# Optimization experiments

Hardware: AMD Instinct MI355X
Metric: run time of the kernel (lower is better)

## Reference

```python
import jax, jax.numpy as jnp
import numpy as np

M_PER_GROUP = 16
EPS = 0.001


def setup_inputs() -> dict:
    key = jax.random.key(0)
    x = jax.random.normal(key, (32, 64, 64, 256), dtype=jnp.float32)
    return {"x": x}


def reference(x) -> jnp.ndarray:
    # x: [B, W, H, C] (NHWC). Training-phase path, decomposition='cholesky', renorm=False.
    b, w, h, c = x.shape
    groups = c // M_PER_GROUP
    n = b * w * h  # samples per channel

    # [C, B*W*H]
    x_flat = jnp.transpose(x, (3, 0, 1, 2)).reshape(c, -1)
    mean = jnp.mean(x_flat, axis=1, keepdims=True)          # [C, 1]
    f = x_flat - mean                                        # [C, N]

    # per-group covariance: [G, m, N] -> [G, m, m]
    fg = f.reshape(groups, M_PER_GROUP, -1)
    denom = jnp.float32(n) - 1.0
    cov = jnp.einsum('gmn,gkn->gmk', fg, fg) / denom
    eye = jnp.eye(M_PER_GROUP, dtype=x.dtype)
    cov = (1.0 - EPS) * cov + EPS * eye
    # NOTE: the original TF code divides by (N-1) a second time after shrinkage;
    # reproduced faithfully here.
    cov = cov / denom

    # batched Cholesky + triangular solve: inv_sqrt = L^{-1}
    chol = jnp.linalg.cholesky(cov)                          # [G, m, m], lower
    inv_sqrt = jax.vmap(
        lambda L: jax.scipy.linalg.solve_triangular(L, eye, lower=True)
    )(chol)                                                  # [G, m, m]

    # whiten: [G, m, m] @ [G, m, N] -> [G, m, N]
    f_hat = jnp.einsum('gmk,gkn->gmn', inv_sqrt, fg)
    out = f_hat.reshape(c, b, w, h)
    return jnp.transpose(out, (1, 2, 3, 0))
```

## Files before the change

kernel.cpp:

```cpp
#include <hip/hip_runtime.h>


#define NROWS   131072
#define DENOMF  131071.0f
#define EPSV    0.001f

#define OFF_INV    0
#define OFF_BIAS   4096
#define OFF_RED1   4352
#define OFF_PART4  217344
#define GSTATS     13312

typedef __attribute__((ext_vector_type(8))) short bf16x8;
typedef __attribute__((ext_vector_type(4))) float f32x4;
typedef __attribute__((ext_vector_type(4))) unsigned int u32x4;

__device__ __forceinline__ unsigned int fbits(float v) {
    return __builtin_bit_cast(unsigned int, v);
}
__device__ __forceinline__ float bfloat(unsigned int u) {
    return __builtin_bit_cast(float, u);
}

__device__ __forceinline__ void gload_lds16(float* lds, const float* g) {
    __builtin_amdgcn_global_load_lds(
        (const __attribute__((address_space(1))) unsigned int*)g,
        (__attribute__((address_space(3))) unsigned int*)lds, 16, 0, 0);
}

struct Row8 { float a, b, c, d, e, f, g, h; };

__device__ __forceinline__ void cvt8(const Row8 r, bf16x8& hv, bf16x8& lv, float& s) {
    s += ((r.a + r.b) + (r.c + r.d)) + ((r.e + r.f) + (r.g + r.h));
    const unsigned int ua = fbits(r.a), ub = fbits(r.b), uc = fbits(r.c), ud = fbits(r.d);
    const unsigned int ue = fbits(r.e), uf = fbits(r.f), ug = fbits(r.g), uh = fbits(r.h);
    u32x4 hp;
    hp.x = (ub & 0xFFFF0000u) | (ua >> 16);
    hp.y = (ud & 0xFFFF0000u) | (uc >> 16);
    hp.z = (uf & 0xFFFF0000u) | (ue >> 16);
    hp.w = (uh & 0xFFFF0000u) | (ug >> 16);
    const float da = r.a - bfloat(ua & 0xFFFF0000u);
    const float db = r.b - bfloat(ub & 0xFFFF0000u);
    const float dc = r.c - bfloat(uc & 0xFFFF0000u);
    const float dd = r.d - bfloat(ud & 0xFFFF0000u);
    const float de = r.e - bfloat(ue & 0xFFFF0000u);
    const float df = r.f - bfloat(uf & 0xFFFF0000u);
    const float dg = r.g - bfloat(ug & 0xFFFF0000u);
    const float dh = r.h - bfloat(uh & 0xFFFF0000u);
    u32x4 lp;
    lp.x = (fbits(db) & 0xFFFF0000u) | (fbits(da) >> 16);
    lp.y = (fbits(dd) & 0xFFFF0000u) | (fbits(dc) >> 16);
    lp.z = (fbits(df) & 0xFFFF0000u) | (fbits(de) >> 16);
    lp.w = (fbits(dh) & 0xFFFF0000u) | (fbits(dg) >> 16);
    hv = __builtin_bit_cast(bf16x8, hp);
    lv = __builtin_bit_cast(bf16x8, lp);
}

__global__ __launch_bounds__(256, 2) void k1_stats(const float* __restrict__ x,
                                                   float* __restrict__ ws, int NB) {
    __shared__ float xt[2][32 * 260];
    const int tid = threadIdx.x;
    const int lane = tid & 63, wv = tid >> 6;
    const int slot = lane >> 4;
    const int TPB = (NROWS / 32) / NB;
    const size_t tile0 = (size_t)blockIdx.x * TPB;

    const int rb = wv * 64 + (lane & 15);
    const int ro0 = (slot * 8 + ((0 + 2 * slot) & 7)) * 260 + rb;
    const int ro1 = (slot * 8 + ((1 + 2 * slot) & 7)) * 260 + rb;
    const int ro2 = (slot * 8 + ((2 + 2 * slot) & 7)) * 260 + rb;
    const int ro3 = (slot * 8 + ((3 + 2 * slot) & 7)) * 260 + rb;
    const int ro4 = (slot * 8 + ((4 + 2 * slot) & 7)) * 260 + rb;
    const int ro5 = (slot * 8 + ((5 + 2 * slot) & 7)) * 260 + rb;
    const int ro6 = (slot * 8 + ((6 + 2 * slot) & 7)) * 260 + rb;
    const int ro7 = (slot * 8 + ((7 + 2 * slot) & 7)) * 260 + rb;

    f32x4 hh0 = {0,0,0,0}, hl0 = {0,0,0,0}, ll0 = {0,0,0,0};
    f32x4 hh1 = {0,0,0,0}, hl1 = {0,0,0,0}, ll1 = {0,0,0,0};
    f32x4 hh2 = {0,0,0,0}, hl2 = {0,0,0,0}, ll2 = {0,0,0,0};
    f32x4 hh3 = {0,0,0,0}, hl3 = {0,0,0,0}, ll3 = {0,0,0,0};
    float s0 = 0.f, s1 = 0.f, s2 = 0.f, s3 = 0.f;

#define STAGE(B, T)                                                           \
    {                                                                         \
        const float* gp = x + ((tile0 + (T)) * 32 + (size_t)(wv * 8)) * 256   \
                            + (size_t)lane * 4;                               \
        float* lb = &xt[B][(wv * 8) * 260];                                   \
        gload_lds16(lb + 0 * 260, gp + 0 * 256);                              \
        gload_lds16(lb + 1 * 260, gp + 1 * 256);                              \
        gload_lds16(lb + 2 * 260, gp + 2 * 256);                              \
        gload_lds16(lb + 3 * 260, gp + 3 * 256);                              \
        gload_lds16(lb + 4 * 260, gp + 4 * 256);                              \
        gload_lds16(lb + 5 * 260, gp + 5 * 256);                              \
        gload_lds16(lb + 6 * 260, gp + 6 * 256);                              \
        gload_lds16(lb + 7 * 260, gp + 7 * 256);                              \
    }
#define PROCG(B, G, AHH, AHL, ALL, S)                                         \
    {                                                                         \
        const float* bp = &xt[B][0];                                          \
        Row8 r;                                                               \
        r.a = bp[ro0 + (G) * 16]; r.b = bp[ro1 + (G) * 16];                   \
        r.c = bp[ro2 + (G) * 16]; r.d = bp[ro3 + (G) * 16];                   \
        r.e = bp[ro4 + (G) * 16]; r.f = bp[ro5 + (G) * 16];                   \
        r.g = bp[ro6 + (G) * 16]; r.h = bp[ro7 + (G) * 16];                   \
        bf16x8 hv, lv;                                                        \
        cvt8(r, hv, lv, S);                                                   \
        AHH = __builtin_amdgcn_mfma_f32_16x16x32_bf16(hv, hv, AHH, 0, 0, 0);  \
        AHL = __builtin_amdgcn_mfma_f32_16x16x32_bf16(hv, lv, AHL, 0, 0, 0);  \
        ALL = __builtin_amdgcn_mfma_f32_16x16x32_bf16(lv, lv, ALL, 0, 0, 0);  \
    }
#define PROC4(B)                                                              \
    PROCG(B, 0, hh0, hl0, ll0, s0);                                           \
    PROCG(B, 1, hh1, hl1, ll1, s1);                                           \
    PROCG(B, 2, hh2, hl2, ll2, s2);                                           \
    PROCG(B, 3, hh3, hl3, ll3, s3);

    STAGE(0, 0);
    for (int t = 0; t < TPB - 1; ++t) {
        __syncthreads();
        STAGE((t + 1) & 1, t + 1);
        PROC4(t & 1);
    }
    __syncthreads();
    PROC4((TPB - 1) & 1);
#undef PROC4
#undef PROCG
#undef STAGE

    const int lane2 = lane;
    float* pb = ws + OFF_PART4 + (size_t)blockIdx.x * GSTATS + (size_t)(wv * 4) * 832;
#define STG(G, AHH, AHL, ALL, S)                                              \
    {                                                                         \
        float* pw = pb + (G) * 832;                                           \
        pw[0 * 64 + lane2]  = AHH[0]; pw[1 * 64 + lane2]  = AHH[1];           \
        pw[2 * 64 + lane2]  = AHH[2]; pw[3 * 64 + lane2]  = AHH[3];           \
        pw[4 * 64 + lane2]  = AHL[0]; pw[5 * 64 + lane2]  = AHL[1];           \
        pw[6 * 64 + lane2]  = AHL[2]; pw[7 * 64 + lane2]  = AHL[3];           \
        pw[8 * 64 + lane2]  = ALL[0]; pw[9 * 64 + lane2]  = ALL[1];           \
        pw[10 * 64 + lane2] = ALL[2]; pw[11 * 64 + lane2] = ALL[3];           \
        pw[12 * 64 + lane2] = S;                                              \
    }
    STG(0, hh0, hl0, ll0, s0);
    STG(1, hh1, hl1, ll1, s1);
    STG(2, hh2, hl2, ll2, s2);
    STG(3, hh3, hl3, ll3, s3);
#undef STG
}

__global__ __launch_bounds__(256, 4) void k2_reduce(float* __restrict__ ws, int NB) {
    const int t = blockIdx.x * 256 + threadIdx.x;
    if (t >= GSTATS) return;
    const int per = NB / 16;
    const float* p = ws + OFF_PART4 + (size_t)(blockIdx.y * per) * GSTATS + t;
    float sum = 0.f;
#pragma unroll 8
    for (int b = 0; b < per; ++b) sum += p[(size_t)b * GSTATS];
    ws[OFF_RED1 + (size_t)blockIdx.y * GSTATS + t] = sum;
}

__global__ void k2_chol(float* __restrict__ ws, int NB) {
    __shared__ float sg[832];
    const int g = blockIdx.x, tid = threadIdx.x;

    for (int e = tid; e < 832; e += 64) {
        float v = 0.f;
#pragma unroll
        for (int y = 0; y < 16; ++y)
            v += ws[OFF_RED1 + (size_t)y * GSTATS + g * 832 + e];
        sg[e] = v;
    }
    __syncthreads();

    const int ii = tid & 15;
    const float inv_denom = 1.0f / DENOMF;
    const float cs_ii = sg[768 + ii] + sg[768 + 16 + ii] +
                        sg[768 + 32 + ii] + sg[768 + 48 + ii];
    const float mu_l = cs_ii * (1.0f / (float)NROWS);

#define GIDX(T, I, J) ((T) * 256 + ((I) & 3) * 64 + ((((I) >> 2)) << 4) + (J))
    float arow[16];
#pragma unroll
    for (int kk = 0; kk < 16; ++kk) {
        float G = sg[GIDX(0, ii, kk)] + sg[GIDX(1, ii, kk)] +
                  sg[GIDX(1, kk, ii)] + sg[GIDX(2, ii, kk)];
        float mu_k = __shfl(mu_l, kk, 64);
        float cv = (G - (float)NROWS * mu_l * mu_k) * inv_denom;
        cv = cv * (1.0f - EPSV) + ((kk == ii) ? EPSV : 0.0f);
        arow[kk] = cv * inv_denom;
    }
#undef GIDX

    float lrow[16];
#pragma unroll
    for (int j = 0; j < 16; ++j) {
        float diag = __shfl(arow[j], j, 64);
        float ljj  = sqrtf(diag);
        float lij  = (ii == j) ? ljj : arow[j] / ljj;
        lrow[j] = lij;
#pragma unroll
        for (int k = j + 1; k < 16; ++k) {
            float lkj = __shfl(lij, k, 64);
            arow[k] = fmaf(-lij, lkj, arow[k]);
        }
    }

    float xcol[16];
#pragma unroll
    for (int i2 = 0; i2 < 16; ++i2) {
        float ssum = (ii == i2) ? 1.0f : 0.0f;
#pragma unroll
        for (int k = 0; k < 16; ++k) {
            if (k < i2) {
                float Lik = __shfl(lrow[k], i2, 64);
                ssum = fmaf(-Lik, xcol[k], ssum);
            }
        }
        float Lii = __shfl(lrow[i2], i2, 64);
        xcol[i2] = (i2 >= ii) ? ssum / Lii : 0.0f;
    }

    float* invg = ws + OFF_INV + g * 256;
#pragma unroll
    for (int i2 = 0; i2 < 16; ++i2) {
        if (tid < 16) invg[i2 * 16 + tid] = xcol[i2];
        float bi = xcol[i2] * mu_l;
        bi += __shfl_xor(bi, 1, 64);
        bi += __shfl_xor(bi, 2, 64);
        bi += __shfl_xor(bi, 4, 64);
        bi += __shfl_xor(bi, 8, 64);
        if (tid == 0) ws[OFF_BIAS + g * 16 + i2] = bi;
    }
}

template <int CTRL>
__device__ __forceinline__ float dpp1(float v) {
    int iv = __builtin_bit_cast(int, v);
    int r = __builtin_amdgcn_update_dpp(iv, iv, CTRL, 0xF, 0xF, false);
    return __builtin_bit_cast(float, r);
}
template <int CTRL>
__device__ __forceinline__ float4 dpp4(float4 v) {
    float4 r;
    r.x = dpp1<CTRL>(v.x);
    r.y = dpp1<CTRL>(v.y);
    r.z = dpp1<CTRL>(v.z);
    r.w = dpp1<CTRL>(v.w);
    return r;
}

#define DOT4(O, A, V) \
    O = fmaf(A.x, V.x, O); O = fmaf(A.y, V.y, O); \
    O = fmaf(A.z, V.z, O); O = fmaf(A.w, V.w, O)

__global__ __launch_bounds__(256, 4) void k3_apply(const float* __restrict__ x,
                                                   const float* __restrict__ ws,
                                                   float* __restrict__ out) {
    const int tid = threadIdx.x, lane = tid & 63, wv = tid >> 6;
    const int q = lane & 3, g = lane >> 2;

    const float* invg = ws + OFF_INV + g * 256;
#define LOADIR(R, M) \
    *reinterpret_cast<const float4*>(invg + (4 * q + (R)) * 16 + 4 * (q ^ (M)))
    float4 ir00 = LOADIR(0, 0), ir01 = LOADIR(0, 1), ir02 = LOADIR(0, 2), ir03 = LOADIR(0, 3);
    float4 ir10 = LOADIR(1, 0), ir11 = LOADIR(1, 1), ir12 = LOADIR(1, 2), ir13 = LOADIR(1, 3);
    float4 ir20 = LOADIR(2, 0), ir21 = LOADIR(2, 1), ir22 = LOADIR(2, 2), ir23 = LOADIR(2, 3);
    float4 ir30 = LOADIR(3, 0), ir31 = LOADIR(3, 1), ir32 = LOADIR(3, 2), ir33 = LOADIR(3, 3);
#undef LOADIR
    float4 b4 = *reinterpret_cast<const float4*>(ws + OFF_BIAS + g * 16 + 4 * q);

    const int rpb   = NROWS / gridDim.x;
    const int iters = rpb / 4;
    const size_t rowbase = (size_t)blockIdx.x * rpb;
    const float4* xp = reinterpret_cast<const float4*>(x) + rowbase * 64 + lane;
    float4*       op = reinterpret_cast<float4*>(out)     + rowbase * 64 + lane;

    float4 cur = xp[(size_t)wv * 64];
    for (int i = 0; i < iters; ++i) {
        const int ip = (i + 1 < iters) ? (i + 1) : (iters - 1);
        float4 nxt = xp[(size_t)(ip * 4 + wv) * 64];

        float4 v0 = cur;
        float4 v1 = dpp4<0xB1>(cur);
        float4 v2 = dpp4<0x4E>(cur);
        float4 v3 = dpp4<0x1B>(cur);

        float o0 = -b4.x, o1 = -b4.y, o2 = -b4.z, o3 = -b4.w;
        DOT4(o0, ir00, v0); DOT4(o0, ir01, v1); DOT4(o0, ir02, v2); DOT4(o0, ir03, v3);
        DOT4(o1, ir10, v0); DOT4(o1, ir11, v1); DOT4(o1, ir12, v2); DOT4(o1, ir13, v3);
        DOT4(o2, ir20, v0); DOT4(o2, ir21, v1); DOT4(o2, ir22, v2); DOT4(o2, ir23, v3);
        DOT4(o3, ir30, v0); DOT4(o3, ir31, v1); DOT4(o3, ir32, v2); DOT4(o3, ir33, v3);

        op[(size_t)(i * 4 + wv) * 64] = make_float4(o0, o1, o2, o3);
        cur = nxt;
    }
}

extern "C" void kernel_launch(void* const* d_in, const int* in_sizes, int n_in,
                              void* d_out, int out_size, void* d_ws, size_t ws_size,
                              hipStream_t stream) {
    const float* x = (const float*)d_in[0];
    float* out = (float*)d_out;
    float* ws  = (float*)d_ws;

    int NB = 128;
    if (ws_size >= (size_t)(OFF_PART4 + 512 * GSTATS) * sizeof(float)) NB = 512;
    else if (ws_size >= (size_t)(OFF_PART4 + 256 * GSTATS) * sizeof(float)) NB = 256;

    k1_stats<<<NB, 256, 0, stream>>>(x, ws, NB);
    dim3 rg((GSTATS + 255) / 256, 16);
    k2_reduce<<<rg, 256, 0, stream>>>(ws, NB);
    k2_chol<<<16, 64, 0, stream>>>(ws, NB);
    k3_apply<<<1024, 256, 0, stream>>>(x, ws, out);
}
```

Baseline: 98.46 us.

## Fuse stats, reduction, Cholesky and apply into one cooperative kernel

```diff
diff --git a/kernel.cpp b/kernel.cpp
--- a/kernel.cpp
+++ b/kernel.cpp
@@ -1,5 +1,8 @@
 #include <hip/hip_runtime.h>
-
+#include <hip/hip_cooperative_groups.h>
+
+
+namespace cg = cooperative_groups;
 
 #define NROWS   131072
 #define DENOMF  131071.0f
@@ -7,8 +10,13 @@
 
 #define OFF_INV    0
 #define OFF_BIAS   4096
-#define OFF_RED1   4352
-#define OFF_PART4  217344
+
+#define M_GS       9216
+#define M_RED1     4352
+#define M_PART     78080
+
+#define OFF_RED1   4900000
+#define OFF_PART4  5113000
 #define GSTATS     13312
 
 typedef __attribute__((ext_vector_type(8))) short bf16x8;
@@ -56,6 +64,260 @@
     lv = __builtin_bit_cast(bf16x8, lp);
 }
 
+template <int CTRL>
+__device__ __forceinline__ float dpp1(float v) {
+    int iv = __builtin_bit_cast(int, v);
+    int r = __builtin_amdgcn_update_dpp(iv, iv, CTRL, 0xF, 0xF, false);
+    return __builtin_bit_cast(float, r);
+}
+template <int CTRL>
+__device__ __forceinline__ float4 dpp4(float4 v) {
+    float4 r;
+    r.x = dpp1<CTRL>(v.x);
+    r.y = dpp1<CTRL>(v.y);
+    r.z = dpp1<CTRL>(v.z);
+    r.w = dpp1<CTRL>(v.w);
+    return r;
+}
+
+#define DOT4(O, A, V) \
+    O = fmaf(A.x, V.x, O); O = fmaf(A.y, V.y, O); \
+    O = fmaf(A.z, V.z, O); O = fmaf(A.w, V.w, O)
+
+__device__ __forceinline__ void chol_from_sg(const float* sg, int g, int tid,
+                                             float* __restrict__ ws) {
+    const int ii = tid & 15;
+    const float inv_denom = 1.0f / DENOMF;
+    const float cs_ii = sg[512 + ii] + sg[512 + 16 + ii] +
+                        sg[512 + 32 + ii] + sg[512 + 48 + ii];
+    const float mu_l = cs_ii * (1.0f / (float)NROWS);
+
+#define GIDX2(T, I, J) ((T) * 256 + ((I) & 3) * 64 + ((((I) >> 2)) << 4) + (J))
+    float arow[16];
+#pragma unroll
+    for (int kk = 0; kk < 16; ++kk) {
+        float G = sg[GIDX2(0, ii, kk)] + sg[GIDX2(1, ii, kk)] + sg[GIDX2(1, kk, ii)];
+        float mu_k = __shfl(mu_l, kk, 64);
+        float cv = (G - (float)NROWS * mu_l * mu_k) * inv_denom;
+        cv = cv * (1.0f - EPSV) + ((kk == ii) ? EPSV : 0.0f);
+        arow[kk] = cv * inv_denom;
+    }
+#undef GIDX2
+
+    float lrow[16];
+#pragma unroll
+    for (int j = 0; j < 16; ++j) {
+        float diag = __shfl(arow[j], j, 64);
+        float ljj  = sqrtf(diag);
+        float lij  = (ii == j) ? ljj : arow[j] / ljj;
+        lrow[j] = lij;
+#pragma unroll
+        for (int k = j + 1; k < 16; ++k) {
+            float lkj = __shfl(lij, k, 64);
+            arow[k] = fmaf(-lij, lkj, arow[k]);
+        }
+    }
+
+    float xcol[16];
+#pragma unroll
+    for (int i2 = 0; i2 < 16; ++i2) {
+        float ssum = (ii == i2) ? 1.0f : 0.0f;
+#pragma unroll
+        for (int k = 0; k < 16; ++k) {
+            if (k < i2) {
+                float Lik = __shfl(lrow[k], i2, 64);
+                ssum = fmaf(-Lik, xcol[k], ssum);
+            }
+        }
+        float Lii = __shfl(lrow[i2], i2, 64);
+        xcol[i2] = (i2 >= ii) ? ssum / Lii : 0.0f;
+    }
+
+    float* invg = ws + OFF_INV + g * 256;
+#pragma unroll
+    for (int i2 = 0; i2 < 16; ++i2) {
+        if (tid < 16) invg[i2 * 16 + tid] = xcol[i2];
+        float bi = xcol[i2] * mu_l;
+        bi += __shfl_xor(bi, 1, 64);
+        bi += __shfl_xor(bi, 2, 64);
+        bi += __shfl_xor(bi, 4, 64);
+        bi += __shfl_xor(bi, 8, 64);
+        if (tid == 0) ws[OFF_BIAS + g * 16 + i2] = bi;
+    }
+}
+
+__global__ __launch_bounds__(256, 2) void mega(const float* __restrict__ x,
+                                               float* __restrict__ ws,
+                                               float* __restrict__ out) {
+    __shared__ float pool[2 * 32 * 260];
+    cg::grid_group grid = cg::this_grid();
+
+    const int tid = threadIdx.x;
+    const int lane = tid & 63, wv = tid >> 6;
+    const int bid = blockIdx.x;
+
+    {
+        float (*xt)[32 * 260] = reinterpret_cast<float (*)[32 * 260]>(pool);
+        const int slot = lane >> 4;
+        const size_t tile0 = (size_t)bid * 8;
+
+        const int rb = wv * 64 + (lane & 15);
+        const int ro0 = (slot * 8 + ((0 + 2 * slot) & 7)) * 260 + rb;
+        const int ro1 = (slot * 8 + ((1 + 2 * slot) & 7)) * 260 + rb;
+        const int ro2 = (slot * 8 + ((2 + 2 * slot) & 7)) * 260 + rb;
+        const int ro3 = (slot * 8 + ((3 + 2 * slot) & 7)) * 260 + rb;
+        const int ro4 = (slot * 8 + ((4 + 2 * slot) & 7)) * 260 + rb;
+        const int ro5 = (slot * 8 + ((5 + 2 * slot) & 7)) * 260 + rb;
+        const int ro6 = (slot * 8 + ((6 + 2 * slot) & 7)) * 260 + rb;
+        const int ro7 = (slot * 8 + ((7 + 2 * slot) & 7)) * 260 + rb;
+
+        f32x4 hh0 = {0,0,0,0}, hl0 = {0,0,0,0}, ll0 = {0,0,0,0};
+        f32x4 hh1 = {0,0,0,0}, hl1 = {0,0,0,0}, ll1 = {0,0,0,0};
+        f32x4 hh2 = {0,0,0,0}, hl2 = {0,0,0,0}, ll2 = {0,0,0,0};
+        f32x4 hh3 = {0,0,0,0}, hl3 = {0,0,0,0}, ll3 = {0,0,0,0};
+        float s0 = 0.f, s1 = 0.f, s2 = 0.f, s3 = 0.f;
+
+#define STAGE(B, T)                                                           \
+        {                                                                     \
+            const float* gp = x + ((tile0 + (T)) * 32 + (size_t)(wv * 8)) * 256 \
+                                + (size_t)lane * 4;                           \
+            float* lb = &xt[B][(wv * 8) * 260];                               \
+            gload_lds16(lb + 0 * 260, gp + 0 * 256);                          \
+            gload_lds16(lb + 1 * 260, gp + 1 * 256);                          \
+            gload_lds16(lb + 2 * 260, gp + 2 * 256);                          \
+            gload_lds16(lb + 3 * 260, gp + 3 * 256);                          \
+            gload_lds16(lb + 4 * 260, gp + 4 * 256);                          \
+            gload_lds16(lb + 5 * 260, gp + 5 * 256);                          \
+            gload_lds16(lb + 6 * 260, gp + 6 * 256);                          \
+            gload_lds16(lb + 7 * 260, gp + 7 * 256);                          \
+        }
+#define PROCG(B, G, AHH, AHL, ALL, S)                                         \
+        {                                                                     \
+            const float* bp = &xt[B][0];                                      \
+            Row8 r;                                                           \
+            r.a = bp[ro0 + (G) * 16]; r.b = bp[ro1 + (G) * 16];               \
+            r.c = bp[ro2 + (G) * 16]; r.d = bp[ro3 + (G) * 16];               \
+            r.e = bp[ro4 + (G) * 16]; r.f = bp[ro5 + (G) * 16];               \
+            r.g = bp[ro6 + (G) * 16]; r.h = bp[ro7 + (G) * 16];               \
+            bf16x8 hv, lv;                                                    \
+            cvt8(r, hv, lv, S);                                               \
+            AHH = __builtin_amdgcn_mfma_f32_16x16x32_bf16(hv, hv, AHH, 0, 0, 0); \
+            AHL = __builtin_amdgcn_mfma_f32_16x16x32_bf16(hv, lv, AHL, 0, 0, 0); \
+            ALL = __builtin_amdgcn_mfma_f32_16x16x32_bf16(lv, lv, ALL, 0, 0, 0); \
+        }
+#define PROC4(B)                                                              \
+        PROCG(B, 0, hh0, hl0, ll0, s0);                                       \
+        PROCG(B, 1, hh1, hl1, ll1, s1);                                       \
+        PROCG(B, 2, hh2, hl2, ll2, s2);                                       \
+        PROCG(B, 3, hh3, hl3, ll3, s3);
+
+        STAGE(0, 0);
+        for (int t = 0; t < 7; ++t) {
+            __syncthreads();
+            STAGE((t + 1) & 1, t + 1);
+            PROC4(t & 1);
+        }
+        __syncthreads();
+        PROC4(1);
+#undef PROC4
+#undef PROCG
+#undef STAGE
+
+        float* pb = ws + M_PART + (size_t)bid * M_GS + (size_t)(wv * 4) * 576;
+#define STG(G, AHH, AHL, ALL, S)                                              \
+        {                                                                     \
+            float* pw = pb + (G) * 576;                                       \
+            pw[0 * 64 + lane] = AHH[0] + ALL[0];                              \
+            pw[1 * 64 + lane] = AHH[1] + ALL[1];                              \
+            pw[2 * 64 + lane] = AHH[2] + ALL[2];                              \
+            pw[3 * 64 + lane] = AHH[3] + ALL[3];                              \
+            pw[4 * 64 + lane] = AHL[0]; pw[5 * 64 + lane] = AHL[1];           \
+            pw[6 * 64 + lane] = AHL[2]; pw[7 * 64 + lane] = AHL[3];           \
+            pw[8 * 64 + lane] = S;                                            \
+        }
+        STG(0, hh0, hl0, ll0, s0);
+        STG(1, hh1, hl1, ll1, s1);
+        STG(2, hh2, hl2, ll2, s2);
+        STG(3, hh3, hl3, ll3, s3);
+#undef STG
+    }
+
+    grid.sync();
+
+    {
+        const int unit = bid * 256 + tid;
+        if (unit < 8 * M_GS) {
+            const int e = unit % M_GS, y = unit / M_GS;
+            const float* p = ws + M_PART + (size_t)(y * 64) * M_GS + e;
+            float sum = 0.f;
+#pragma unroll 8
+            for (int b = 0; b < 64; ++b) sum += p[(size_t)b * M_GS];
+            ws[M_RED1 + (size_t)y * M_GS + e] = sum;
+        }
+    }
+
+    grid.sync();
+
+    if (bid < 16) {
+        float* sgrp = pool;
+        for (int e = tid; e < 576; e += 256) {
+            float v = 0.f;
+#pragma unroll
+            for (int y = 0; y < 8; ++y)
+                v += ws[M_RED1 + (size_t)y * M_GS + bid * 576 + e];
+            sgrp[e] = v;
+        }
+        __syncthreads();
+        if (tid < 64) chol_from_sg(sgrp, bid, tid, ws);
+    }
+
+    grid.sync();
+
+    {
+        const int q = lane & 3, g = lane >> 2;
+        const float* invg = ws + OFF_INV + g * 256;
+#define LOADIR(R, M) \
+        *reinterpret_cast<const float4*>(invg + (4 * q + (R)) * 16 + 4 * (q ^ (M)))
+        float4 ir00 = LOADIR(0, 0), ir01 = LOADIR(0, 1), ir02 = LOADIR(0, 2), ir03 = LOADIR(0, 3);
+        float4 ir10 = LOADIR(1, 0), ir11 = LOADIR(1, 1), ir12 = LOADIR(1, 2), ir13 = LOADIR(1, 3);
+        float4 ir20 = LOADIR(2, 0), ir21 = LOADIR(2, 1), ir22 = LOADIR(2, 2), ir23 = LOADIR(2, 3);
+        float4 ir30 = LOADIR(3, 0), ir31 = LOADIR(3, 1), ir32 = LOADIR(3, 2), ir33 = LOADIR(3, 3);
+#undef LOADIR
+        float4 b4 = *reinterpret_cast<const float4*>(ws + OFF_BIAS + g * 16 + 4 * q);
+
+        const size_t rowbase = (size_t)bid * 256;
+        const float4* xp = reinterpret_cast<const float4*>(x) + rowbase * 64 + lane;
+        float4*       op = reinterpret_cast<float4*>(out)     + rowbase * 64 + lane;
+
+#define APPLY1(V, OIDX)                                                       \
+        {                                                                     \
+            float4 v0 = (V);                                                  \
+            float4 v1 = dpp4<0xB1>(v0);                                       \
+            float4 v2 = dpp4<0x4E>(v0);                                       \
+            float4 v3 = dpp4<0x1B>(v0);                                       \
+            float o0 = -b4.x, o1 = -b4.y, o2 = -b4.z, o3 = -b4.w;             \
+            DOT4(o0, ir00, v0); DOT4(o0, ir01, v1); DOT4(o0, ir02, v2); DOT4(o0, ir03, v3); \
+            DOT4(o1, ir10, v0); DOT4(o1, ir11, v1); DOT4(o1, ir12, v2); DOT4(o1, ir13, v3); \
+            DOT4(o2, ir20, v0); DOT4(o2, ir21, v1); DOT4(o2, ir22, v2); DOT4(o2, ir23, v3); \
+            DOT4(o3, ir30, v0); DOT4(o3, ir31, v1); DOT4(o3, ir32, v2); DOT4(o3, ir33, v3); \
+            op[(size_t)(OIDX) * 64] = make_float4(o0, o1, o2, o3);            \
+        }
+
+        float4 c0 = xp[(size_t)(2 * wv) * 64];
+        float4 c1 = xp[(size_t)(2 * wv + 1) * 64];
+        for (int i = 0; i < 32; ++i) {
+            const int pn = (i + 1 < 32) ? ((i + 1) * 4 + wv) : (31 * 4 + wv);
+            float4 n0 = xp[(size_t)(2 * pn) * 64];
+            float4 n1 = xp[(size_t)(2 * pn + 1) * 64];
+            const int p = i * 4 + wv;
+            APPLY1(c0, 2 * p);
+            APPLY1(c1, 2 * p + 1);
+            c0 = n0; c1 = n1;
+        }
+#undef APPLY1
+    }
+}
+
 __global__ __launch_bounds__(256, 2) void k1_stats(const float* __restrict__ x,
                                                    float* __restrict__ ws, int NB) {
     __shared__ float xt[2][32 * 260];
@@ -127,18 +389,17 @@
 #undef PROCG
 #undef STAGE
 
-    const int lane2 = lane;
     float* pb = ws + OFF_PART4 + (size_t)blockIdx.x * GSTATS + (size_t)(wv * 4) * 832;
 #define STG(G, AHH, AHL, ALL, S)                                              \
     {                                                                         \
         float* pw = pb + (G) * 832;                                           \
-        pw[0 * 64 + lane2]  = AHH[0]; pw[1 * 64 + lane2]  = AHH[1];           \
-        pw[2 * 64 + lane2]  = AHH[2]; pw[3 * 64 + lane2]  = AHH[3];           \
-        pw[4 * 64 + lane2]  = AHL[0]; pw[5 * 64 + lane2]  = AHL[1];           \
-        pw[6 * 64 + lane2]  = AHL[2]; pw[7 * 64 + lane2]  = AHL[3];           \
-        pw[8 * 64 + lane2]  = ALL[0]; pw[9 * 64 + lane2]  = ALL[1];           \
-        pw[10 * 64 + lane2] = ALL[2]; pw[11 * 64 + lane2] = ALL[3];           \
-        pw[12 * 64 + lane2] = S;                                              \
+        pw[0 * 64 + lane]  = AHH[0]; pw[1 * 64 + lane]  = AHH[1];             \
+        pw[2 * 64 + lane]  = AHH[2]; pw[3 * 64 + lane]  = AHH[3];             \
+        pw[4 * 64 + lane]  = AHL[0]; pw[5 * 64 + lane]  = AHL[1];             \
+        pw[6 * 64 + lane]  = AHL[2]; pw[7 * 64 + lane]  = AHL[3];             \
+        pw[8 * 64 + lane]  = ALL[0]; pw[9 * 64 + lane]  = ALL[1];             \
+        pw[10 * 64 + lane] = ALL[2]; pw[11 * 64 + lane] = ALL[3];             \
+        pw[12 * 64 + lane] = S;                                               \
     }
     STG(0, hh0, hl0, ll0, s0);
     STG(1, hh1, hl1, ll1, s1);
@@ -159,7 +420,7 @@
 }
 
 __global__ void k2_chol(float* __restrict__ ws, int NB) {
-    __shared__ float sg[832];
+    __shared__ float sg2[832];
     const int g = blockIdx.x, tid = threadIdx.x;
 
     for (int e = tid; e < 832; e += 64) {
@@ -167,90 +428,19 @@
 #pragma unroll
         for (int y = 0; y < 16; ++y)
             v += ws[OFF_RED1 + (size_t)y * GSTATS + g * 832 + e];
-        sg[e] = v;
+        sg2[e] = v;
     }
     __syncthreads();
 
-    const int ii = tid & 15;
-    const float inv_denom = 1.0f / DENOMF;
-    const float cs_ii = sg[768 + ii] + sg[768 + 16 + ii] +
-                        sg[768 + 32 + ii] + sg[768 + 48 + ii];
-    const float mu_l = cs_ii * (1.0f / (float)NROWS);
-
-#define GIDX(T, I, J) ((T) * 256 + ((I) & 3) * 64 + ((((I) >> 2)) << 4) + (J))
-    float arow[16];
-#pragma unroll
-    for (int kk = 0; kk < 16; ++kk) {
-        float G = sg[GIDX(0, ii, kk)] + sg[GIDX(1, ii, kk)] +
-                  sg[GIDX(1, kk, ii)] + sg[GIDX(2, ii, kk)];
-        float mu_k = __shfl(mu_l, kk, 64);
-        float cv = (G - (float)NROWS * mu_l * mu_k) * inv_denom;
-        cv = cv * (1.0f - EPSV) + ((kk == ii) ? EPSV : 0.0f);
-        arow[kk] = cv * inv_denom;
-    }
-#undef GIDX
-
-    float lrow[16];
-#pragma unroll
-    for (int j = 0; j < 16; ++j) {
-        float diag = __shfl(arow[j], j, 64);
-        float ljj  = sqrtf(diag);
-        float lij  = (ii == j) ? ljj : arow[j] / ljj;
-        lrow[j] = lij;
-#pragma unroll
-        for (int k = j + 1; k < 16; ++k) {
-            float lkj = __shfl(lij, k, 64);
-            arow[k] = fmaf(-lij, lkj, arow[k]);
-        }
-    }
-
-    float xcol[16];
-#pragma unroll
-    for (int i2 = 0; i2 < 16; ++i2) {
-        float ssum = (ii == i2) ? 1.0f : 0.0f;
-#pragma unroll
-        for (int k = 0; k < 16; ++k) {
-            if (k < i2) {
-                float Lik = __shfl(lrow[k], i2, 64);
-                ssum = fmaf(-Lik, xcol[k], ssum);
-            }
-        }
-        float Lii = __shfl(lrow[i2], i2, 64);
-        xcol[i2] = (i2 >= ii) ? ssum / Lii : 0.0f;
-    }
-
-    float* invg = ws + OFF_INV + g * 256;
-#pragma unroll
-    for (int i2 = 0; i2 < 16; ++i2) {
-        if (tid < 16) invg[i2 * 16 + tid] = xcol[i2];
-        float bi = xcol[i2] * mu_l;
-        bi += __shfl_xor(bi, 1, 64);
-        bi += __shfl_xor(bi, 2, 64);
-        bi += __shfl_xor(bi, 4, 64);
-        bi += __shfl_xor(bi, 8, 64);
-        if (tid == 0) ws[OFF_BIAS + g * 16 + i2] = bi;
-    }
-}
-
-template <int CTRL>
-__device__ __forceinline__ float dpp1(float v) {
-    int iv = __builtin_bit_cast(int, v);
-    int r = __builtin_amdgcn_update_dpp(iv, iv, CTRL, 0xF, 0xF, false);
-    return __builtin_bit_cast(float, r);
-}
-template <int CTRL>
-__device__ __forceinline__ float4 dpp4(float4 v) {
-    float4 r;
-    r.x = dpp1<CTRL>(v.x);
-    r.y = dpp1<CTRL>(v.y);
-    r.z = dpp1<CTRL>(v.z);
-    r.w = dpp1<CTRL>(v.w);
-    return r;
-}
-
-#define DOT4(O, A, V) \
-    O = fmaf(A.x, V.x, O); O = fmaf(A.y, V.y, O); \
-    O = fmaf(A.z, V.z, O); O = fmaf(A.w, V.w, O)
+    __shared__ float sg[576];
+    for (int e = tid; e < 256; e += 64) {
+        sg[e] = sg2[e] + sg2[512 + e];
+        sg[256 + e] = sg2[256 + e];
+    }
+    for (int e = tid; e < 64; e += 64) sg[512 + e] = sg2[768 + e];
+    __syncthreads();
+    if (tid < 64) chol_from_sg(sg, g, tid, ws);
+}
 
 __global__ __launch_bounds__(256, 4) void k3_apply(const float* __restrict__ x,
                                                    const float* __restrict__ ws,
@@ -302,6 +492,11 @@
     float* out = (float*)d_out;
     float* ws  = (float*)d_ws;
 
+    void* args[] = {(void*)&x, (void*)&ws, (void*)&out};
+    hipError_t e = hipLaunchCooperativeKernel((const void*)mega, dim3(512),
+                                              dim3(256), args, 0, stream);
+    if (e == hipSuccess) return;
+
     int NB = 128;
     if (ws_size >= (size_t)(OFF_PART4 + 512 * GSTATS) * sizeof(float)) NB = 512;
     else if (ws_size >= (size_t)(OFF_PART4 + 256 * GSTATS) * sizeof(float)) NB = 256;
```

Result: slower. 253.8 us (+157.8%).
